# Performance work log

Hardware: AMD Instinct MI355X
Metric: run time of the kernel (lower is better)

Reference implementation:

```python
import jax, jax.numpy as jnp
import numpy as np

DIM = 1024
HEADS = 16
DIM_HEAD = 64
INNER = HEADS * DIM_HEAD  # 1024
MLP = 4096


def setup_inputs() -> dict:
    key = jax.random.key(0)
    ks = jax.random.split(key, 10)
    s = lambda k, shape, fan: jax.random.normal(k, shape, jnp.float32) * (fan ** -0.5)
    return {
        "x": jax.random.normal(ks[0], (4, 2048, DIM), jnp.float32),
        "ln1_g": jnp.ones((DIM,), jnp.float32),
        "ln1_b": jnp.zeros((DIM,), jnp.float32),
        "w_qkv": s(ks[1], (DIM, 3 * INNER), DIM),
        "w_out": s(ks[2], (INNER, DIM), INNER),
        "b_out": jnp.zeros((DIM,), jnp.float32),
        "ln2_g": jnp.ones((DIM,), jnp.float32),
        "ln2_b": jnp.zeros((DIM,), jnp.float32),
        "w1": s(ks[3], (DIM, MLP), DIM),
        "b1": jnp.zeros((MLP,), jnp.float32),
        "w2": s(ks[4], (MLP, DIM), MLP),
        "b2": jnp.zeros((DIM,), jnp.float32),
    }


def layernorm(x, g, b, eps=1e-5):
    mu = jnp.mean(x, axis=-1, keepdims=True)
    var = jnp.mean(jnp.square(x - mu), axis=-1, keepdims=True)
    return (x - mu) * jax.lax.rsqrt(var + eps) * g + b


def reference(x, ln1_g, ln1_b, w_qkv, w_out, b_out, ln2_g, ln2_b, w1, b1, w2, b2):
    b, n, d = x.shape
    h, dh = HEADS, DIM_HEAD
    scale = dh ** -0.5

    # Attention sub-block (pre-LN)
    xn = layernorm(x, ln1_g, ln1_b)
    qkv = xn @ w_qkv                                   # [b, n, 3*inner]
    q, k, v = jnp.split(qkv, 3, axis=-1)
    to_heads = lambda t: t.reshape(b, n, h, dh).transpose(0, 2, 1, 3)  # [b,h,n,dh]
    q, k, v = to_heads(q), to_heads(k), to_heads(v)
    dots = jnp.einsum('bhqd,bhkd->bhqk', q, k) * scale  # [b,h,n,n]
    attn = jax.nn.softmax(dots, axis=-1)
    out = jnp.einsum('bhqk,bhkd->bhqd', attn, v)        # [b,h,n,dh]
    out = out.transpose(0, 2, 1, 3).reshape(b, n, h * dh)
    x = x + out @ w_out + b_out

    # MLP sub-block (pre-LN)
    xn = layernorm(x, ln2_g, ln2_b)
    hdn = jax.nn.gelu(xn @ w1 + b1, approximate=False)
    x = x + hdn @ w2 + b2
    return x
```

## Files before the change

kernel.cpp:

```cpp
#include <hip/hip_runtime.h>
#include <hip/hip_bf16.h>
#include <math.h>

#define DIM   1024
#define HEADS 16
#define DH    64
#define SEQ   2048
#define BATCH 4
#define ROWS  (BATCH * SEQ)
#define MLP   4096
#define QKV3  (3 * DIM)

typedef __bf16    bf16x8 __attribute__((ext_vector_type(8)));
typedef __bf16    bf16x4 __attribute__((ext_vector_type(4)));
typedef float     f32x4  __attribute__((ext_vector_type(4)));
typedef unsigned int u32x2 __attribute__((ext_vector_type(2)));

__device__ inline void store_out(float* p, float v)           { *p = v; }
__device__ inline void store_out(__hip_bfloat16* p, float v)  { *p = __float2bfloat16(v); }

#define GLP(p) ((const __attribute__((address_space(1))) void*)(p))
#define LDP(p) ((__attribute__((address_space(3))) void*)(p))

__device__ inline float fast_exp2(float x) {
#if __has_builtin(__builtin_amdgcn_exp2f)
    return __builtin_amdgcn_exp2f(x);
#else
    return __expf(x * 0.69314718056f);
#endif
}

__device__ inline float fast_rcp(float x) {
#if __has_builtin(__builtin_amdgcn_rcpf)
    return __builtin_amdgcn_rcpf(x);
#else
    return 1.f / x;
#endif
}

__global__ __launch_bounds__(256) void ln_kernel(
    const float* __restrict__ x,
    const float* __restrict__ g,
    const float* __restrict__ b,
    __hip_bfloat16* __restrict__ y)
{
    const int row = blockIdx.x;
    const int tid = threadIdx.x;
    __shared__ float red[256];

    const float* xr = x + (size_t)row * DIM;
    float vals[4];
    float s = 0.f;
#pragma unroll
    for (int i = 0; i < 4; ++i) {
        vals[i] = xr[tid + i * 256];
        s += vals[i];
    }
    red[tid] = s; __syncthreads();
    for (int t = 128; t > 0; t >>= 1) { if (tid < t) red[tid] += red[tid + t]; __syncthreads(); }
    const float mu = red[0] * (1.f / DIM);
    __syncthreads();

    float vs = 0.f;
#pragma unroll
    for (int i = 0; i < 4; ++i) { float d = vals[i] - mu; vs += d * d; }
    red[tid] = vs; __syncthreads();
    for (int t = 128; t > 0; t >>= 1) { if (tid < t) red[tid] += red[tid + t]; __syncthreads(); }
    const float rstd = rsqrtf(red[0] * (1.f / DIM) + 1e-5f);

#pragma unroll
    for (int i = 0; i < 4; ++i) {
        const int c = tid + i * 256;
        float o = (vals[i] - mu) * rstd * g[c] + b[c];
        y[(size_t)row * DIM + c] = __float2bfloat16(o);
    }
}

__global__ __launch_bounds__(256) void transpose_w_kernel(
    const float* __restrict__ B, __bf16* __restrict__ BT,
    int Nfull, int r0, int c0, int Ksub)
{
    const int kb = blockIdx.x, nb = blockIdx.y;
    __shared__ float T[32][33];
    const int t  = threadIdx.x;
    const int r  = t >> 3;
    const int cq = (t & 7) * 4;

    f32x4 v = *(const f32x4*)(B + (size_t)(r0 + kb * 32 + r) * Nfull + c0 + nb * 32 + cq);
    T[r][cq] = v[0]; T[r][cq + 1] = v[1]; T[r][cq + 2] = v[2]; T[r][cq + 3] = v[3];
    __syncthreads();

    bf16x4 o;
#pragma unroll
    for (int i = 0; i < 4; ++i) o[i] = (__bf16)T[cq + i][r];
    *(bf16x4*)(BT + (size_t)(nb * 32 + r) * Ksub + kb * 32 + cq) = o;
}

template <typename OutT>
__global__ __launch_bounds__(512, 3) void gemm_bt_kernel(
    const __bf16* __restrict__ A,
    const __bf16* __restrict__ BT,
    const float* __restrict__ bias,
    const float* __restrict__ res,
    OutT* __restrict__ C,
    int M, int N, int K, int do_gelu)
{
    __shared__ __align__(16) __bf16 As[2][256 * 32];
    __shared__ __align__(16) __bf16 Bs[2][128 * 32];

    const int tid  = threadIdx.x;
    const int lane = tid & 63;
    const int w    = tid >> 6;
    const int q    = lane >> 4;
    const int c    = lane & 15;
    const int mw   = (w >> 1) * 64;
    const int nw   = (w & 1) * 64;

    const int rowTile = blockIdx.y * 256;
    const int colTile = blockIdx.x * 128;

    const int sRow = tid >> 2;
    const int sK   = (tid & 3) * 8;
    const __bf16* Ap0 = A  + (size_t)(rowTile + sRow) * K + sK;
    const __bf16* Ap1 = A  + (size_t)(rowTile + 128 + sRow) * K + sK;
    const __bf16* Bp  = BT + (size_t)(colTile + sRow) * K + sK;
    const int wd = w * 512;

    f32x4 acc[4][4];
#pragma unroll
    for (int i = 0; i < 4; ++i)
#pragma unroll
        for (int j = 0; j < 4; ++j) acc[i][j] = (f32x4){0.f, 0.f, 0.f, 0.f};

    __builtin_amdgcn_global_load_lds(GLP(Ap0), LDP(&As[0][wd]),        16, 0, 0);
    __builtin_amdgcn_global_load_lds(GLP(Ap1), LDP(&As[0][4096 + wd]), 16, 0, 0);
    __builtin_amdgcn_global_load_lds(GLP(Bp ), LDP(&Bs[0][wd]),        16, 0, 0);
    __syncthreads();

    for (int k0 = 0; k0 < K; k0 += 32) {
        const int cur = (k0 >> 5) & 1;
        if (k0 + 32 < K) {
            const int nxt = cur ^ 1;
            __builtin_amdgcn_global_load_lds(GLP(Ap0 + k0 + 32), LDP(&As[nxt][wd]),        16, 0, 0);
            __builtin_amdgcn_global_load_lds(GLP(Ap1 + k0 + 32), LDP(&As[nxt][4096 + wd]), 16, 0, 0);
            __builtin_amdgcn_global_load_lds(GLP(Bp  + k0 + 32), LDP(&Bs[nxt][wd]),        16, 0, 0);
        }

        bf16x8 af[4], bf[4];
#pragma unroll
        for (int mt = 0; mt < 4; ++mt)
            af[mt] = *(const bf16x8*)(&As[cur][(mw + mt * 16 + c) * 32 + q * 8]);
#pragma unroll
        for (int nt = 0; nt < 4; ++nt)
            bf[nt] = *(const bf16x8*)(&Bs[cur][(nw + nt * 16 + c) * 32 + q * 8]);

#pragma unroll
        for (int mt = 0; mt < 4; ++mt)
#pragma unroll
            for (int nt = 0; nt < 4; ++nt)
                acc[mt][nt] = __builtin_amdgcn_mfma_f32_16x16x32_bf16(af[mt], bf[nt], acc[mt][nt], 0, 0, 0);

        __syncthreads();
    }

#pragma unroll
    for (int nt = 0; nt < 4; ++nt) {
        const int col = colTile + nw + nt * 16 + c;
        const float bv = bias ? bias[col] : 0.f;
#pragma unroll
        for (int mt = 0; mt < 4; ++mt) {
#pragma unroll
            for (int r = 0; r < 4; ++r) {
                const int row = rowTile + mw + mt * 16 + q * 4 + r;
                float v = acc[mt][nt][r] + bv;
                if (do_gelu) {
                    const float y2 = fminf(1.5957691216057308f * v * (1.f + 0.044715f * v * v), 80.f);
                    const float e  = __expf(y2);
                    v = v * e * fast_rcp(e + 1.f);
                }
                if (res) v += res[(size_t)row * N + col];
                store_out(&C[(size_t)row * N + col], v);
            }
        }
    }
}

#define KB  64
#define QB  256
#define KTP 72
#define VTP 72
#define NT  (SEQ / KB)
#define NEG_M0_LOG2E  (-11.541560327111707f)
#define QSCALE_LOG2E  (0.18033688011112043f)

__global__ __launch_bounds__(256, 2) void flash_attn_kernel(
    const __hip_bfloat16* __restrict__ qkv,
    __hip_bfloat16* __restrict__ out)
{
    const int tid  = threadIdx.x;
    const int w    = tid >> 6;
    const int lane = tid & 63;
    const int quad = lane >> 4;
    const int c    = lane & 15;

    const int h = blockIdx.y;
    const int b = blockIdx.z;
    const size_t base = (size_t)b * SEQ;
    const int qbase = blockIdx.x * QB + w * 64;

    __shared__ __align__(16) __bf16 Kt[KB * KTP];
    __shared__ __align__(16) __bf16 Vt[DH * VTP];

    const __bf16* qkvb = (const __bf16*)qkv;

    bf16x8 aq[4][2];
#pragma unroll
    for (int qg = 0; qg < 4; ++qg)
#pragma unroll
        for (int kk = 0; kk < 2; ++kk) {
            bf16x8 t = *(const bf16x8*)(qkvb + (base + qbase + qg * 16 + c) * QKV3
                                        + h * DH + kk * 32 + quad * 8);
#pragma unroll
            for (int j = 0; j < 8; ++j) aq[qg][kk][j] = (__bf16)(QSCALE_LOG2E * (float)t[j]);
        }

    bf16x8 onesv;
#pragma unroll
    for (int j = 0; j < 8; ++j) onesv[j] = (__bf16)1.0f;

    f32x4 o[4][4];
#pragma unroll
    for (int qg = 0; qg < 4; ++qg)
#pragma unroll
        for (int ch = 0; ch < 4; ++ch) o[qg][ch] = (f32x4){0.f, 0.f, 0.f, 0.f};
    f32x4 ol[4] = {{0,0,0,0},{0,0,0,0},{0,0,0,0},{0,0,0,0}};

    const int sR = tid >> 3;
    const int sD = (tid & 7) * 8;
    const __bf16* Kg = qkvb + (base + sR) * QKV3 + DIM + h * DH + sD;

    const int vm = tid & 7;
    const int d0 = (tid >> 3) * 2;
    const __bf16* Vg = qkvb + (base + 8 * vm) * QKV3 + 2 * DIM + h * DH + d0;
    const int bpos = 32 * (vm >> 2) + 16 * (vm & 1) + 4 * ((vm >> 1) & 1);

    bf16x8 kA, kB_;
    unsigned vv[8];
    kA  = *(const bf16x8*)(Kg);
    kB_ = *(const bf16x8*)(Kg + (size_t)32 * QKV3);
#pragma unroll
    for (int j = 0; j < 8; ++j)
        vv[j] = *(const unsigned*)(Vg + (size_t)j * QKV3);

    for (int kt = 0; kt < NT; ++kt) {
        *(bf16x8*)(&Kt[sR * KTP + sD])        = kA;
        *(bf16x8*)(&Kt[(sR + 32) * KTP + sD]) = kB_;
        {
            const unsigned lo01 = (vv[0] & 0xFFFFu) | (vv[1] << 16);
            const unsigned lo23 = (vv[2] & 0xFFFFu) | (vv[3] << 16);
            const unsigned lo45 = (vv[4] & 0xFFFFu) | (vv[5] << 16);
            const unsigned lo67 = (vv[6] & 0xFFFFu) | (vv[7] << 16);
            const unsigned hi01 = (vv[0] >> 16) | (vv[1] & 0xFFFF0000u);
            const unsigned hi23 = (vv[2] >> 16) | (vv[3] & 0xFFFF0000u);
            const unsigned hi45 = (vv[4] >> 16) | (vv[5] & 0xFFFF0000u);
            const unsigned hi67 = (vv[6] >> 16) | (vv[7] & 0xFFFF0000u);
            *(u32x2*)(&Vt[(d0    ) * VTP + bpos])     = (u32x2){lo01, lo23};
            *(u32x2*)(&Vt[(d0    ) * VTP + bpos + 8]) = (u32x2){lo45, lo67};
            *(u32x2*)(&Vt[(d0 + 1) * VTP + bpos])     = (u32x2){hi01, hi23};
            *(u32x2*)(&Vt[(d0 + 1) * VTP + bpos + 8]) = (u32x2){hi45, hi67};
        }
        __syncthreads();

        if (kt + 1 < NT) {
            const size_t koff = (size_t)(kt + 1) * KB * QKV3;
            kA  = *(const bf16x8*)(Kg + koff);
            kB_ = *(const bf16x8*)(Kg + koff + (size_t)32 * QKV3);
#pragma unroll
            for (int j = 0; j < 8; ++j)
                vv[j] = *(const unsigned*)(Vg + koff + (size_t)j * QKV3);
        }

        bf16x8 kf[4][2];
#pragma unroll
        for (int kg = 0; kg < 4; ++kg)
#pragma unroll
            for (int kk = 0; kk < 2; ++kk)
                kf[kg][kk] = *(const bf16x8*)(&Kt[(kg * 16 + c) * KTP + kk * 32 + quad * 8]);

        bf16x8 ap[4][2];
#pragma unroll
        for (int qg = 0; qg < 4; ++qg) {
            f32x4 st[4];
#pragma unroll
            for (int kg = 0; kg < 4; ++kg)
                st[kg] = (f32x4){NEG_M0_LOG2E, NEG_M0_LOG2E, NEG_M0_LOG2E, NEG_M0_LOG2E};
            __builtin_amdgcn_s_setprio(1);
#pragma unroll
            for (int kg = 0; kg < 4; ++kg)
#pragma unroll
                for (int kk = 0; kk < 2; ++kk)
                    st[kg] = __builtin_amdgcn_mfma_f32_16x16x32_bf16(kf[kg][kk], aq[qg][kk], st[kg], 0, 0, 0);
            __builtin_amdgcn_s_setprio(0);

#pragma unroll
            for (int kg = 0; kg < 4; ++kg)
#pragma unroll
                for (int r = 0; r < 4; ++r)
                    ap[qg][kg >> 1][(kg & 1) * 4 + r] = (__bf16)fast_exp2(st[kg][r]);
        }

        __builtin_amdgcn_s_setprio(1);
#pragma unroll
        for (int qg = 0; qg < 4; ++qg) {
            ol[qg] = __builtin_amdgcn_mfma_f32_16x16x32_bf16(ap[qg][0], onesv, ol[qg], 0, 0, 0);
            ol[qg] = __builtin_amdgcn_mfma_f32_16x16x32_bf16(ap[qg][1], onesv, ol[qg], 0, 0, 0);
        }
#pragma unroll
        for (int h2 = 0; h2 < 2; ++h2)
#pragma unroll
            for (int ch = 0; ch < 4; ++ch) {
                bf16x8 bv = *(const bf16x8*)(&Vt[(ch * 16 + c) * VTP + h2 * 32 + quad * 8]);
#pragma unroll
                for (int qg = 0; qg < 4; ++qg)
                    o[qg][ch] = __builtin_amdgcn_mfma_f32_16x16x32_bf16(ap[qg][h2], bv, o[qg][ch], 0, 0, 0);
            }
        __builtin_amdgcn_s_setprio(0);
        __syncthreads();
    }

#pragma unroll
    for (int qg = 0; qg < 4; ++qg) {
#pragma unroll
        for (int r = 0; r < 4; ++r) {
            const float inv = 1.f / ol[qg][r];
            const size_t row = base + qbase + qg * 16 + quad * 4 + r;
#pragma unroll
            for (int ch = 0; ch < 4; ++ch)
                out[row * DIM + h * DH + ch * 16 + c] = __float2bfloat16(o[qg][ch][r] * inv);
        }
    }
}

extern "C" void kernel_launch(void* const* d_in, const int* in_sizes, int n_in,
                              void* d_out, int out_size, void* d_ws, size_t ws_size,
                              hipStream_t stream)
{
    const float* x     = (const float*)d_in[0];
    const float* ln1_g = (const float*)d_in[1];
    const float* ln1_b = (const float*)d_in[2];
    const float* w_qkv = (const float*)d_in[3];
    const float* w_out = (const float*)d_in[4];
    const float* b_out = (const float*)d_in[5];
    const float* ln2_g = (const float*)d_in[6];
    const float* ln2_b = (const float*)d_in[7];
    const float* w1    = (const float*)d_in[8];
    const float* b1    = (const float*)d_in[9];
    const float* w2    = (const float*)d_in[10];
    const float* b2    = (const float*)d_in[11];
    float* out = (float*)d_out;

    char* ws = (char*)d_ws;
    const size_t MiB = 1024 * 1024;
    __hip_bfloat16* X   = (__hip_bfloat16*)(ws);
    __bf16*         wT  = (__bf16*)(ws + 16 * MiB);
    __hip_bfloat16* qkv = (__hip_bfloat16*)(ws + 24 * MiB);
    __bf16*         hdn = (__bf16*)(ws + 24 * MiB);

    dim3 blk(256);
    dim3 blk512(512);

    transpose_w_kernel<<<dim3(DIM / 32, QKV3 / 32), blk, 0, stream>>>(w_qkv, wT, QKV3, 0, 0, DIM);
    ln_kernel<<<dim3(ROWS), blk, 0, stream>>>(x, ln1_g, ln1_b, X);
    gemm_bt_kernel<__hip_bfloat16><<<dim3(QKV3 / 128, ROWS / 256), blk512, 0, stream>>>(
        (const __bf16*)X, wT, nullptr, nullptr, qkv, ROWS, QKV3, DIM, 0);
    flash_attn_kernel<<<dim3(SEQ / QB, HEADS, BATCH), blk, 0, stream>>>(qkv, X);
    transpose_w_kernel<<<dim3(DIM / 32, DIM / 32), blk, 0, stream>>>(w_out, wT, DIM, 0, 0, DIM);
    gemm_bt_kernel<float><<<dim3(DIM / 128, ROWS / 256), blk512, 0, stream>>>(
        (const __bf16*)X, wT, b_out, x, out, ROWS, DIM, DIM, 0);
    ln_kernel<<<dim3(ROWS), blk, 0, stream>>>(out, ln2_g, ln2_b, X);

    transpose_w_kernel<<<dim3(DIM / 32, 2048 / 32), blk, 0, stream>>>(w1, wT, MLP, 0, 0, DIM);
    gemm_bt_kernel<__hip_bfloat16><<<dim3(2048 / 128, ROWS / 256), blk512, 0, stream>>>(
        (const __bf16*)X, wT, b1, nullptr, (__hip_bfloat16*)hdn, ROWS, 2048, DIM, 1);
    transpose_w_kernel<<<dim3(2048 / 32, DIM / 32), blk, 0, stream>>>(w2, wT, DIM, 0, 0, 2048);
    gemm_bt_kernel<float><<<dim3(DIM / 128, ROWS / 256), blk512, 0, stream>>>(
        hdn, wT, b2, out, out, ROWS, DIM, 2048, 0);

    transpose_w_kernel<<<dim3(DIM / 32, 2048 / 32), blk, 0, stream>>>(w1, wT, MLP, 0, 2048, DIM);
    gemm_bt_kernel<__hip_bfloat16><<<dim3(2048 / 128, ROWS / 256), blk512, 0, stream>>>(
        (const __bf16*)X, wT, b1 + 2048, nullptr, (__hip_bfloat16*)hdn, ROWS, 2048, DIM, 1);
    transpose_w_kernel<<<dim3(2048 / 32, DIM / 32), blk, 0, stream>>>(w2, wT, DIM, 2048, 0, 2048);
    gemm_bt_kernel<float><<<dim3(DIM / 128, ROWS / 256), blk512, 0, stream>>>(
        hdn, wT, nullptr, out, out, ROWS, DIM, 2048, 0);
}
```

Measured before the change: 602.2 us.

## Triple-buffer GEMM LDS pipeline with one barrier per step and XCD-aware tile swizzle

The GEMM moves from double to triple buffering of the LDS tiles, so global loads are issued two K-steps ahead. It also replaces two __syncthreads per iteration with one vmcnt wait plus a barrier. Blocks are launched on a 1D grid and remapped so consecutive tiles land on the same XCD (round-robin over 8), which should improve L2 reuse of A and B. The cost is 50% more LDS per block (144KB for 3 blocks? actually 72KB per block), which may limit occupancy despite the launch_bounds hint rising to 4, and the swizzle assumes the grid size is divisible by 8.

```diff
diff --git a/kernel.cpp b/kernel.cpp
--- a/kernel.cpp
+++ b/kernel.cpp
@@ -97,7 +97,7 @@
 }
 
 template <typename OutT>
-__global__ __launch_bounds__(512, 3) void gemm_bt_kernel(
+__global__ __launch_bounds__(512, 4) void gemm_bt_kernel(
     const __bf16* __restrict__ A,
     const __bf16* __restrict__ BT,
     const float* __restrict__ bias,
@@ -105,8 +105,8 @@
     OutT* __restrict__ C,
     int M, int N, int K, int do_gelu)
 {
-    __shared__ __align__(16) __bf16 As[2][256 * 32];
-    __shared__ __align__(16) __bf16 Bs[2][128 * 32];
+    __shared__ __align__(16) __bf16 As[3][256 * 32];
+    __shared__ __align__(16) __bf16 Bs[3][128 * 32];
 
     const int tid  = threadIdx.x;
     const int lane = tid & 63;
@@ -116,8 +116,12 @@
     const int mw   = (w >> 1) * 64;
     const int nw   = (w & 1) * 64;
 
-    const int rowTile = blockIdx.y * 256;
-    const int colTile = blockIdx.x * 128;
+    const int nwg = gridDim.x;
+    const int cpx = nwg >> 3;
+    const int swz = ((int)blockIdx.x & 7) * cpx + ((int)blockIdx.x >> 3);
+    const int colTiles = N >> 7;
+    const int rowTile  = (swz / colTiles) * 256;
+    const int colTile  = (swz % colTiles) * 128;
 
     const int sRow = tid >> 2;
     const int sK   = (tid & 3) * 8;
@@ -132,18 +136,29 @@
 #pragma unroll
         for (int j = 0; j < 4; ++j) acc[i][j] = (f32x4){0.f, 0.f, 0.f, 0.f};
 
+    const int nt = K >> 5;
+
     __builtin_amdgcn_global_load_lds(GLP(Ap0), LDP(&As[0][wd]),        16, 0, 0);
     __builtin_amdgcn_global_load_lds(GLP(Ap1), LDP(&As[0][4096 + wd]), 16, 0, 0);
     __builtin_amdgcn_global_load_lds(GLP(Bp ), LDP(&Bs[0][wd]),        16, 0, 0);
-    __syncthreads();
-
-    for (int k0 = 0; k0 < K; k0 += 32) {
-        const int cur = (k0 >> 5) & 1;
-        if (k0 + 32 < K) {
-            const int nxt = cur ^ 1;
-            __builtin_amdgcn_global_load_lds(GLP(Ap0 + k0 + 32), LDP(&As[nxt][wd]),        16, 0, 0);
-            __builtin_amdgcn_global_load_lds(GLP(Ap1 + k0 + 32), LDP(&As[nxt][4096 + wd]), 16, 0, 0);
-            __builtin_amdgcn_global_load_lds(GLP(Bp  + k0 + 32), LDP(&Bs[nxt][wd]),        16, 0, 0);
+    __builtin_amdgcn_global_load_lds(GLP(Ap0 + 32), LDP(&As[1][wd]),        16, 0, 0);
+    __builtin_amdgcn_global_load_lds(GLP(Ap1 + 32), LDP(&As[1][4096 + wd]), 16, 0, 0);
+    __builtin_amdgcn_global_load_lds(GLP(Bp  + 32), LDP(&Bs[1][wd]),        16, 0, 0);
+
+    for (int t = 0; t < nt; ++t) {
+        const int cur = t % 3;
+
+        asm volatile("s_waitcnt vmcnt(3)" ::: "memory");
+        if (t + 1 == nt) asm volatile("s_waitcnt vmcnt(0)" ::: "memory");
+        __builtin_amdgcn_s_barrier();
+        __builtin_amdgcn_sched_barrier(0);
+
+        if (t + 2 < nt) {
+            const int nb = (t + 2) % 3;
+            const int ko = (t + 2) * 32;
+            __builtin_amdgcn_global_load_lds(GLP(Ap0 + ko), LDP(&As[nb][wd]),        16, 0, 0);
+            __builtin_amdgcn_global_load_lds(GLP(Ap1 + ko), LDP(&As[nb][4096 + wd]), 16, 0, 0);
+            __builtin_amdgcn_global_load_lds(GLP(Bp  + ko), LDP(&Bs[nb][wd]),        16, 0, 0);
         }
 
         bf16x8 af[4], bf[4];
@@ -151,28 +166,26 @@
         for (int mt = 0; mt < 4; ++mt)
             af[mt] = *(const bf16x8*)(&As[cur][(mw + mt * 16 + c) * 32 + q * 8]);
 #pragma unroll
-        for (int nt = 0; nt < 4; ++nt)
-            bf[nt] = *(const bf16x8*)(&Bs[cur][(nw + nt * 16 + c) * 32 + q * 8]);
+        for (int nt2 = 0; nt2 < 4; ++nt2)
+            bf[nt2] = *(const bf16x8*)(&Bs[cur][(nw + nt2 * 16 + c) * 32 + q * 8]);
 
 #pragma unroll
         for (int mt = 0; mt < 4; ++mt)
 #pragma unroll
-            for (int nt = 0; nt < 4; ++nt)
-                acc[mt][nt] = __builtin_amdgcn_mfma_f32_16x16x32_bf16(af[mt], bf[nt], acc[mt][nt], 0, 0, 0);
-
-        __syncthreads();
-    }
-
-#pragma unroll
-    for (int nt = 0; nt < 4; ++nt) {
-        const int col = colTile + nw + nt * 16 + c;
+            for (int nt2 = 0; nt2 < 4; ++nt2)
+                acc[mt][nt2] = __builtin_amdgcn_mfma_f32_16x16x32_bf16(af[mt], bf[nt2], acc[mt][nt2], 0, 0, 0);
+    }
+
+#pragma unroll
+    for (int nt2 = 0; nt2 < 4; ++nt2) {
+        const int col = colTile + nw + nt2 * 16 + c;
         const float bv = bias ? bias[col] : 0.f;
 #pragma unroll
         for (int mt = 0; mt < 4; ++mt) {
 #pragma unroll
             for (int r = 0; r < 4; ++r) {
                 const int row = rowTile + mw + mt * 16 + q * 4 + r;
-                float v = acc[mt][nt][r] + bv;
+                float v = acc[mt][nt2][r] + bv;
                 if (do_gelu) {
                     const float y2 = fminf(1.5957691216057308f * v * (1.f + 0.044715f * v * v), 80.f);
                     const float e  = __expf(y2);
@@ -371,25 +384,25 @@
 
     transpose_w_kernel<<<dim3(DIM / 32, QKV3 / 32), blk, 0, stream>>>(w_qkv, wT, QKV3, 0, 0, DIM);
     ln_kernel<<<dim3(ROWS), blk, 0, stream>>>(x, ln1_g, ln1_b, X);
-    gemm_bt_kernel<__hip_bfloat16><<<dim3(QKV3 / 128, ROWS / 256), blk512, 0, stream>>>(
+    gemm_bt_kernel<__hip_bfloat16><<<dim3((QKV3 / 128) * (ROWS / 256)), blk512, 0, stream>>>(
         (const __bf16*)X, wT, nullptr, nullptr, qkv, ROWS, QKV3, DIM, 0);
     flash_attn_kernel<<<dim3(SEQ / QB, HEADS, BATCH), blk, 0, stream>>>(qkv, X);
     transpose_w_kernel<<<dim3(DIM / 32, DIM / 32), blk, 0, stream>>>(w_out, wT, DIM, 0, 0, DIM);
-    gemm_bt_kernel<float><<<dim3(DIM / 128, ROWS / 256), blk512, 0, stream>>>(
+    gemm_bt_kernel<float><<<dim3((DIM / 128) * (ROWS / 256)), blk512, 0, stream>>>(
         (const __bf16*)X, wT, b_out, x, out, ROWS, DIM, DIM, 0);
     ln_kernel<<<dim3(ROWS), blk, 0, stream>>>(out, ln2_g, ln2_b, X);
 
     transpose_w_kernel<<<dim3(DIM / 32, 2048 / 32), blk, 0, stream>>>(w1, wT, MLP, 0, 0, DIM);
-    gemm_bt_kernel<__hip_bfloat16><<<dim3(2048 / 128, ROWS / 256), blk512, 0, stream>>>(
+    gemm_bt_kernel<__hip_bfloat16><<<dim3((2048 / 128) * (ROWS / 256)), blk512, 0, stream>>>(
         (const __bf16*)X, wT, b1, nullptr, (__hip_bfloat16*)hdn, ROWS, 2048, DIM, 1);
     transpose_w_kernel<<<dim3(2048 / 32, DIM / 32), blk, 0, stream>>>(w2, wT, DIM, 0, 0, 2048);
-    gemm_bt_kernel<float><<<dim3(DIM / 128, ROWS / 256), blk512, 0, stream>>>(
+    gemm_bt_kernel<float><<<dim3((DIM / 128) * (ROWS / 256)), blk512, 0, stream>>>(
         hdn, wT, b2, out, out, ROWS, DIM, 2048, 0);
 
     transpose_w_kernel<<<dim3(DIM / 32, 2048 / 32), blk, 0, stream>>>(w1, wT, MLP, 0, 2048, DIM);
-    gemm_bt_kernel<__hip_bfloat16><<<dim3(2048 / 128, ROWS / 256), blk512, 0, stream>>>(
+    gemm_bt_kernel<__hip_bfloat16><<<dim3((2048 / 128) * (ROWS / 256)), blk512, 0, stream>>>(
         (const __bf16*)X, wT, b1 + 2048, nullptr, (__hip_bfloat16*)hdn, ROWS, 2048, DIM, 1);
     transpose_w_kernel<<<dim3(2048 / 32, DIM / 32), blk, 0, stream>>>(w2, wT, DIM, 2048, 0, 2048);
-    gemm_bt_kernel<float><<<dim3(DIM / 128, ROWS / 256), blk512, 0, stream>>>(
+    gemm_bt_kernel<float><<<dim3((DIM / 128) * (ROWS / 256)), blk512, 0, stream>>>(
         hdn, wT, nullptr, out, out, ROWS, DIM, 2048, 0);
 }
```

Result: no change. 603.4 us (+0.2%).
